# Performance work log

Measured on AMD Instinct MI355X. Metric: run time of the kernel, lower is better.

## Reference

```python
import math
import jax, jax.numpy as jnp
import numpy as np

S = 16384          # number of tokens
M = 1024           # model_dim
E = 64             # num_experts
CAPACITY_FACTOR = 1.0
MIN_CAPACITY = 8


def setup_inputs() -> dict:
    key = jax.random.key(0)
    kx, kw = jax.random.split(key)
    x = jax.random.normal(kx, (S, M), dtype=jnp.float32)
    wg_weight = jax.random.normal(kw, (E, M), dtype=jnp.float32) * 0.02  # torch Linear weight [out, in]
    return {"x": x, "wg_weight": wg_weight}


def reference(x, wg_weight):
    s, _ = x.shape
    e = wg_weight.shape[0]
    # gate linear (no bias), fp32 as in the torch module
    logits = jnp.einsum('sm,em->se', x, wg_weight)
    gates = jax.nn.softmax(logits, axis=1)

    # capacity (static: shapes + python floats)
    capacity = int(math.ceil(s / e * CAPACITY_FACTOR))
    capacity = max(capacity, MIN_CAPACITY)

    # top-1 expert per token
    indices1_s = jnp.argmax(gates, axis=1)                      # [s]
    mask1 = jax.nn.one_hot(indices1_s, e, dtype=jnp.int32)      # [s, e]
    exp_counts = jnp.sum(mask1, axis=0)                         # [e]

    alpha = jnp.max(gates, axis=1, keepdims=True)               # [s, 1]

    # load-balancing aux loss
    me = jnp.mean(gates, axis=0)
    ce = jnp.mean(mask1.astype(jnp.float32), axis=0)
    l_aux = jnp.sum(me * ce) * e

    # random tie-break for capacity selection (use_rts=True)
    rts_key = jax.random.key(42)
    mask1_rand = mask1.astype(jnp.float32) * jax.random.uniform(rts_key, (s, e), dtype=jnp.float32)

    # keep top-`capacity` tokens per expert (topk along token dim)
    top_idx = jax.lax.top_k(mask1_rand.T, capacity)[1].T        # [capacity, e]
    keep = jnp.zeros((s, e), dtype=jnp.int32).at[top_idx, jnp.arange(e)[None, :]].set(1)
    mask1 = mask1 * keep

    # slot assignment within each expert's capacity buffer
    locations1 = jnp.cumsum(mask1, axis=0) - 1                  # [s, e]
    locations1_s = jnp.sum(locations1 * mask1, axis=1)          # [s]

    mask1_float = mask1.astype(jnp.float32)
    gates = gates * mask1_float
    locations1_sc = jax.nn.one_hot(locations1_s, capacity, dtype=jnp.float32)  # [s, c]

    combine_weights = jnp.einsum('se,sc->sec', gates, locations1_sc)           # [s, e, c]
    dispatch_mask = combine_weights.astype(bool)

    return (l_aux, combine_weights, dispatch_mask, exp_counts, alpha)
```

## Files before the change

### kernel.cpp

```cpp
#include <hip/hip_runtime.h>
#include <stdint.h>

#define S_TOK 16384
#define MDIM  1024
#define NEXP  64
#define CAP   256

static constexpr size_t SEC    = (size_t)S_TOK * NEXP * CAP;
static constexpr size_t CW_OFF = 1;
static constexpr size_t DM_OFF = 1 + SEC;
static constexpr size_t EC_OFF = 1 + 2 * SEC;
static constexpr size_t AL_OFF = EC_OFF + NEXP;

__device__ __forceinline__ uint32_t rotl32(uint32_t x, int n) {
  return (x << n) | (x >> (32 - n));
}

__device__ float jax_u01(uint32_t i) {
  const uint32_t half = (uint32_t)(S_TOK * NEXP / 2);
  uint32_t x0, x1;
  const bool hi = (i >= half);
  if (hi) { x0 = i - half; x1 = i; } else { x0 = i; x1 = i + half; }
  const uint32_t ks0 = 0u;
  const uint32_t ks1 = 42u;
  const uint32_t ks2 = 0x1BD11BDAu ^ ks0 ^ ks1;
  x0 += ks0; x1 += ks1;
#define TF_R(r) { x0 += x1; x1 = rotl32(x1, (r)); x1 ^= x0; }
  TF_R(13) TF_R(15) TF_R(26) TF_R(6)
  x0 += ks1; x1 += ks2 + 1u;
  TF_R(17) TF_R(29) TF_R(16) TF_R(24)
  x0 += ks2; x1 += ks0 + 2u;
  TF_R(13) TF_R(15) TF_R(26) TF_R(6)
  x0 += ks0; x1 += ks1 + 3u;
  TF_R(17) TF_R(29) TF_R(16) TF_R(24)
  x0 += ks1; x1 += ks2 + 4u;
  TF_R(13) TF_R(15) TF_R(26) TF_R(6)
  x0 += ks2; x1 += ks0 + 5u;
#undef TF_R
  const uint32_t bits = hi ? x1 : x0;
  return __uint_as_float((bits >> 9) | 0x3F800000u) - 1.0f;
}

__global__ __launch_bounds__(256) void k_gate(
    const float* __restrict__ x, const float* __restrict__ wg,
    float* __restrict__ out,
    int* __restrict__ expert_ws, float* __restrict__ uval_ws,
    float* __restrict__ alpha_ws, float* __restrict__ colsum_ws,
    int* __restrict__ counts_ws)
{
  __shared__ float xs[64][68];
  __shared__ float wsh[64][68];

  const int tid  = threadIdx.x;
  const int tok0 = blockIdx.x * 64;
  const int tr   = tid >> 4;
  const int tc   = tid & 15;

  float acc[4][4] = {};

  for (int kc = 0; kc < MDIM; kc += 64) {
    __syncthreads();
#pragma unroll
    for (int i = 0; i < 4; ++i) {
      const int r = (tid >> 4) + 16 * i;
      const int f = tid & 15;
      const float4 xv = *(const float4*)(x  + (size_t)(tok0 + r) * MDIM + kc + f * 4);
      *(float4*)(&xs[r][f * 4]) = xv;
      const float4 wv = *(const float4*)(wg + (size_t)r * MDIM + kc + f * 4);
      const int fs = f ^ ((r >> 2) & 7);
      *(float4*)(&wsh[r][fs * 4]) = wv;
    }
    __syncthreads();
#pragma unroll
    for (int k4 = 0; k4 < 16; ++k4) {
      float4 a[4], b[4];
#pragma unroll
      for (int i = 0; i < 4; ++i)
        a[i] = *(const float4*)(&xs[tr * 4 + i][k4 * 4]);
#pragma unroll
      for (int j = 0; j < 4; ++j) {
        const int e  = tc * 4 + j;
        const int fs = k4 ^ ((e >> 2) & 7);
        b[j] = *(const float4*)(&wsh[e][fs * 4]);
      }
#pragma unroll
      for (int i = 0; i < 4; ++i)
#pragma unroll
        for (int j = 0; j < 4; ++j)
          acc[i][j] += a[i].x * b[j].x + a[i].y * b[j].y +
                       a[i].z * b[j].z + a[i].w * b[j].w;
    }
  }

  __syncthreads();
#pragma unroll
  for (int i = 0; i < 4; ++i)
#pragma unroll
    for (int j = 0; j < 4; ++j)
      xs[tr * 4 + i][tc * 4 + j] = acc[i][j];
  __syncthreads();

  if (tid < 64) {
    const int t = tid;
    float mx = -3.0e38f; int am = 0;
    for (int e = 0; e < NEXP; ++e) {
      const float v = xs[t][e];
      if (v > mx) { mx = v; am = e; }
    }
    float sum = 0.f;
    for (int e = 0; e < NEXP; ++e) {
      const float g = expf(xs[t][e] - mx);
      xs[t][e] = g;
      sum += g;
    }
    const float inv = 1.0f / sum;
    for (int e = 0; e < NEXP; ++e) xs[t][e] *= inv;

    const int s = tok0 + t;
    expert_ws[s] = am;
    alpha_ws[s]  = inv;
    out[AL_OFF + s] = inv;
    uval_ws[s] = jax_u01((uint32_t)s * (uint32_t)NEXP + (uint32_t)am);
    atomicAdd(&counts_ws[am], 1);
  }
  __syncthreads();

  if (tid < 64) {
    float s = 0.f;
    for (int t = 0; t < 64; ++t) s += xs[t][tid];
    colsum_ws[(size_t)blockIdx.x * 64 + tid] = s;
  }
}

__global__ __launch_bounds__(256) void k_select(
    const int* __restrict__ expert_ws, const float* __restrict__ uval_ws,
    const float* __restrict__ alpha_ws, float* __restrict__ out)
{
  __shared__ float su[1024];
  __shared__ int   sidx[1024];
  __shared__ int   skept[1024];
  __shared__ int   scnt;

  const int e   = blockIdx.x;
  const int tid = threadIdx.x;
  if (tid == 0) scnt = 0;
  __syncthreads();

  for (int s = tid; s < S_TOK; s += 256) {
    if (expert_ws[s] == e) {
      const int p = atomicAdd(&scnt, 1);
      if (p < 1024) { su[p] = uval_ws[s]; sidx[p] = s; }
    }
  }
  __syncthreads();
  const int n = min(scnt, 1024);

  for (int t = tid; t < n; t += 256) {
    int keep = 1;
    if (n > CAP) {
      const float ut = su[t];
      const int   it = sidx[t];
      int r = 0;
      for (int j = 0; j < n; ++j) {
        const float uj = su[j];
        r += (uj > ut) || (uj == ut && sidx[j] < it);
      }
      keep = (r < CAP);
    }
    skept[t] = keep;
  }
  __syncthreads();

  for (int t = tid; t < n; t += 256) {
    if (!skept[t]) continue;
    const int it = sidx[t];
    int slot = 0;
    for (int j = 0; j < n; ++j) slot += (skept[j] && (sidx[j] < it));
    const size_t base = CW_OFF + ((size_t)it * NEXP + e) * CAP + (size_t)slot;
    out[base]       = alpha_ws[it];
    out[base + SEC] = 1.0f;
  }
}

__global__ __launch_bounds__(64) void k_final(
    const float* __restrict__ colsum_ws, const int* __restrict__ counts_ws,
    float* __restrict__ out)
{
  const int e = threadIdx.x;
  float s = 0.f;
  for (int b = 0; b < 256; ++b) s += colsum_ws[(size_t)b * 64 + e];
  const float me = s / (float)S_TOK;
  const int   cnt = counts_ws[e];
  const float ce = (float)cnt / (float)S_TOK;
  out[EC_OFF + e] = (float)cnt;
  float v = me * ce;
#pragma unroll
  for (int off = 32; off > 0; off >>= 1) v += __shfl_down(v, off, 64);
  if (e == 0) out[0] = v * (float)NEXP;
}

extern "C" void kernel_launch(void* const* d_in, const int* in_sizes, int n_in,
                              void* d_out, int out_size, void* d_ws, size_t ws_size,
                              hipStream_t stream)
{
  const float* x  = (const float*)d_in[0];
  const float* wg = (const float*)d_in[1];
  float* out = (float*)d_out;

  char* ws = (char*)d_ws;
  int*   expert_ws = (int*)  (ws + 0);
  float* uval_ws   = (float*)(ws + 65536);
  float* alpha_ws  = (float*)(ws + 131072);
  float* colsum_ws = (float*)(ws + 196608);
  int*   counts_ws = (int*)  (ws + 262144);

  hipMemsetAsync(d_out, 0, (size_t)out_size * sizeof(float), stream);
  hipMemsetAsync(counts_ws, 0, NEXP * sizeof(int), stream);

  k_gate  <<<S_TOK / 64, 256, 0, stream>>>(x, wg, out, expert_ws, uval_ws,
                                           alpha_ws, colsum_ws, counts_ws);
  k_select<<<NEXP,       256, 0, stream>>>(expert_ws, uval_ws, alpha_ws, out);
  k_final <<<1,           64, 0, stream>>>(colsum_ws, counts_ws, out);
}
```

Before: 489.4 us.

## Replace full output memset and scatter with a single streaming dense write kernel

Drops the hipMemsetAsync of the whole output and the scattered writes. k_select now only records each token's flat slot index, and a new k_write kernel streams every row of combine_weights and dispatch_mask once with nontemporal vector stores, putting the value in place at the kept slot. Expert counts are taken from k_select's per-expert tally instead of global atomics, and the aux-loss reduction is folded into k_write. This removes one extra pass over the roughly 2 GB output, at the cost of handling the misaligned row offset with scalar edge stores.

Measured after the change: 741.0 us. +51.4%, slower.

```diff
diff --git a/kernel.cpp b/kernel.cpp
--- a/kernel.cpp
+++ b/kernel.cpp
@@ -8,9 +8,10 @@
 
 static constexpr size_t SEC    = (size_t)S_TOK * NEXP * CAP;
 static constexpr size_t CW_OFF = 1;
-static constexpr size_t DM_OFF = 1 + SEC;
 static constexpr size_t EC_OFF = 1 + 2 * SEC;
 static constexpr size_t AL_OFF = EC_OFF + NEXP;
+
+typedef float floatx4 __attribute__((ext_vector_type(4)));
 
 __device__ __forceinline__ uint32_t rotl32(uint32_t x, int n) {
   return (x << n) | (x >> (32 - n));
@@ -45,8 +46,7 @@
     const float* __restrict__ x, const float* __restrict__ wg,
     float* __restrict__ out,
     int* __restrict__ expert_ws, float* __restrict__ uval_ws,
-    float* __restrict__ alpha_ws, float* __restrict__ colsum_ws,
-    int* __restrict__ counts_ws)
+    float* __restrict__ alpha_ws, float* __restrict__ colsum_ws)
 {
   __shared__ float xs[64][68];
   __shared__ float wsh[64][68];
@@ -121,7 +121,6 @@
     alpha_ws[s]  = inv;
     out[AL_OFF + s] = inv;
     uval_ws[s] = jax_u01((uint32_t)s * (uint32_t)NEXP + (uint32_t)am);
-    atomicAdd(&counts_ws[am], 1);
   }
   __syncthreads();
 
@@ -134,7 +133,8 @@
 
 __global__ __launch_bounds__(256) void k_select(
     const int* __restrict__ expert_ws, const float* __restrict__ uval_ws,
-    const float* __restrict__ alpha_ws, float* __restrict__ out)
+    int* __restrict__ slotj_ws, int* __restrict__ counts_ws,
+    float* __restrict__ out)
 {
   __shared__ float su[1024];
   __shared__ int   sidx[1024];
@@ -154,6 +154,11 @@
   }
   __syncthreads();
   const int n = min(scnt, 1024);
+
+  if (tid == 0) {
+    counts_ws[e] = scnt;
+    out[EC_OFF + e] = (float)scnt;
+  }
 
   for (int t = tid; t < n; t += 256) {
     int keep = 1;
@@ -172,31 +177,55 @@
   __syncthreads();
 
   for (int t = tid; t < n; t += 256) {
-    if (!skept[t]) continue;
     const int it = sidx[t];
-    int slot = 0;
-    for (int j = 0; j < n; ++j) slot += (skept[j] && (sidx[j] < it));
-    const size_t base = CW_OFF + ((size_t)it * NEXP + e) * CAP + (size_t)slot;
-    out[base]       = alpha_ws[it];
-    out[base + SEC] = 1.0f;
-  }
-}
-
-__global__ __launch_bounds__(64) void k_final(
+    int sj = -1;
+    if (skept[t]) {
+      int slot = 0;
+      for (int j = 0; j < n; ++j) slot += (skept[j] && (sidx[j] < it));
+      sj = e * CAP + slot;
+    }
+    slotj_ws[it] = sj;
+  }
+}
+
+__global__ __launch_bounds__(256) void k_write(
+    const int* __restrict__ slotj_ws, const float* __restrict__ alpha_ws,
     const float* __restrict__ colsum_ws, const int* __restrict__ counts_ws,
     float* __restrict__ out)
 {
-  const int e = threadIdx.x;
-  float s = 0.f;
-  for (int b = 0; b < 256; ++b) s += colsum_ws[(size_t)b * 64 + e];
-  const float me = s / (float)S_TOK;
-  const int   cnt = counts_ws[e];
-  const float ce = (float)cnt / (float)S_TOK;
-  out[EC_OFF + e] = (float)cnt;
-  float v = me * ce;
-#pragma unroll
-  for (int off = 32; off > 0; off >>= 1) v += __shfl_down(v, off, 64);
-  if (e == 0) out[0] = v * (float)NEXP;
+  const int bid = blockIdx.x;
+  const int tid = threadIdx.x;
+  const int s   = bid & (S_TOK - 1);
+  const int r   = bid >> 14;
+
+  const size_t f0 = CW_OFF + (size_t)r * SEC + (size_t)s * 16384;
+  const int    tj = slotj_ws[s];
+  const float  val = r ? 1.0f : alpha_ws[s];
+
+  if (tid < 3)       out[f0 + tid]   = (tj == tid)   ? val : 0.0f;
+  else if (tid == 3) out[f0 + 16383] = (tj == 16383) ? val : 0.0f;
+
+  float* const rowp = out + f0 + 3;
+#pragma unroll 4
+  for (int q = tid; q < 4095; q += 256) {
+    const int jbase = 3 + q * 4;
+    floatx4 v = (floatx4)(0.f);
+    const int d = tj - jbase;
+    if ((unsigned)d < 4u) v[d] = val;
+    __builtin_nontemporal_store(v, (floatx4*)(rowp + q * 4));
+  }
+
+  if (bid == 0 && tid < 64) {
+    const int e = tid;
+    float cs = 0.f;
+    for (int b = 0; b < 256; ++b) cs += colsum_ws[(size_t)b * 64 + e];
+    const float me = cs / (float)S_TOK;
+    const float ce = (float)counts_ws[e] / (float)S_TOK;
+    float v = me * ce;
+#pragma unroll
+    for (int off = 32; off > 0; off >>= 1) v += __shfl_down(v, off, 64);
+    if (e == 0) out[0] = v * (float)NEXP;
+  }
 }
 
 extern "C" void kernel_launch(void* const* d_in, const int* in_sizes, int n_in,
@@ -213,12 +242,12 @@
   float* alpha_ws  = (float*)(ws + 131072);
   float* colsum_ws = (float*)(ws + 196608);
   int*   counts_ws = (int*)  (ws + 262144);
-
-  hipMemsetAsync(d_out, 0, (size_t)out_size * sizeof(float), stream);
-  hipMemsetAsync(counts_ws, 0, NEXP * sizeof(int), stream);
+  int*   slotj_ws  = (int*)  (ws + 262400);
 
   k_gate  <<<S_TOK / 64, 256, 0, stream>>>(x, wg, out, expert_ws, uval_ws,
-                                           alpha_ws, colsum_ws, counts_ws);
-  k_select<<<NEXP,       256, 0, stream>>>(expert_ws, uval_ws, alpha_ws, out);
-  k_final <<<1,           64, 0, stream>>>(colsum_ws, counts_ws, out);
-}
+                                           alpha_ws, colsum_ws);
+  k_select<<<NEXP,       256, 0, stream>>>(expert_ws, uval_ws, slotj_ws,
+                                           counts_ws, out);
+  k_write <<<2 * S_TOK,  256, 0, stream>>>(slotj_ws, alpha_ws, colsum_ws,
+                                           counts_ws, out);
+}
```

## Fuse output zero-fill into gate kernel and derive expert counts in select

Applied to the files above, without the earlier changes.

Drops the full-output hipMemsetAsync and the counts memset. The gate kernel gets extra blocks that zero the combine and dispatch regions with aligned float4 stores, so the fill runs alongside the gating GEMM blocks. Per-expert counts are now written by k_select from its per-expert gather count rather than by global atomics. The zero-fill stays bound by memory bandwidth, so any gain depends on overlapping it with the GEMM, on saving a launch, and on the custom fill matching the bandwidth of the driver memset.

Measured after the change: 533.6 us. 9.0% more time.

```diff
diff --git a/kernel.cpp b/kernel.cpp
--- a/kernel.cpp
+++ b/kernel.cpp
@@ -8,9 +8,11 @@
 
 static constexpr size_t SEC    = (size_t)S_TOK * NEXP * CAP;
 static constexpr size_t CW_OFF = 1;
-static constexpr size_t DM_OFF = 1 + SEC;
 static constexpr size_t EC_OFF = 1 + 2 * SEC;
 static constexpr size_t AL_OFF = EC_OFF + NEXP;
+
+static constexpr int    NFILLB = 32768;
+static constexpr size_t NQ4    = 134217727;
 
 __device__ __forceinline__ uint32_t rotl32(uint32_t x, int n) {
   return (x << n) | (x >> (32 - n));
@@ -41,17 +43,34 @@
   return __uint_as_float((bits >> 9) | 0x3F800000u) - 1.0f;
 }
 
-__global__ __launch_bounds__(256) void k_gate(
+__global__ __launch_bounds__(256) void k_gate_fill(
     const float* __restrict__ x, const float* __restrict__ wg,
     float* __restrict__ out,
     int* __restrict__ expert_ws, float* __restrict__ uval_ws,
-    float* __restrict__ alpha_ws, float* __restrict__ colsum_ws,
-    int* __restrict__ counts_ws)
+    float* __restrict__ alpha_ws, float* __restrict__ colsum_ws)
 {
   __shared__ float xs[64][68];
   __shared__ float wsh[64][68];
 
-  const int tid  = threadIdx.x;
+  const int tid = threadIdx.x;
+
+  if (blockIdx.x >= 256) {
+    const int fb = blockIdx.x - 256;
+    const size_t qbase = (size_t)fb * 4096;
+    const float4 z = make_float4(0.f, 0.f, 0.f, 0.f);
+    float* const p4 = out + 4;
+#pragma unroll 4
+    for (int i = 0; i < 16; ++i) {
+      const size_t q = qbase + (size_t)(i * 256 + tid);
+      if (q < NQ4) *(float4*)(p4 + q * 4) = z;
+    }
+    if (fb == 0) {
+      if (tid < 3)       out[1 + tid]          = 0.f;
+      else if (tid == 3) out[1 + 2 * SEC - 1]  = 0.f;
+    }
+    return;
+  }
+
   const int tok0 = blockIdx.x * 64;
   const int tr   = tid >> 4;
   const int tc   = tid & 15;
@@ -121,7 +140,6 @@
     alpha_ws[s]  = inv;
     out[AL_OFF + s] = inv;
     uval_ws[s] = jax_u01((uint32_t)s * (uint32_t)NEXP + (uint32_t)am);
-    atomicAdd(&counts_ws[am], 1);
   }
   __syncthreads();
 
@@ -134,7 +152,8 @@
 
 __global__ __launch_bounds__(256) void k_select(
     const int* __restrict__ expert_ws, const float* __restrict__ uval_ws,
-    const float* __restrict__ alpha_ws, float* __restrict__ out)
+    const float* __restrict__ alpha_ws, int* __restrict__ counts_ws,
+    float* __restrict__ out)
 {
   __shared__ float su[1024];
   __shared__ int   sidx[1024];
@@ -154,6 +173,11 @@
   }
   __syncthreads();
   const int n = min(scnt, 1024);
+
+  if (tid == 0) {
+    counts_ws[e] = scnt;
+    out[EC_OFF + e] = (float)scnt;
+  }
 
   for (int t = tid; t < n; t += 256) {
     int keep = 1;
@@ -190,9 +214,7 @@
   float s = 0.f;
   for (int b = 0; b < 256; ++b) s += colsum_ws[(size_t)b * 64 + e];
   const float me = s / (float)S_TOK;
-  const int   cnt = counts_ws[e];
-  const float ce = (float)cnt / (float)S_TOK;
-  out[EC_OFF + e] = (float)cnt;
+  const float ce = (float)counts_ws[e] / (float)S_TOK;
   float v = me * ce;
 #pragma unroll
   for (int off = 32; off > 0; off >>= 1) v += __shfl_down(v, off, 64);
@@ -214,11 +236,9 @@
   float* colsum_ws = (float*)(ws + 196608);
   int*   counts_ws = (int*)  (ws + 262144);
 
-  hipMemsetAsync(d_out, 0, (size_t)out_size * sizeof(float), stream);
-  hipMemsetAsync(counts_ws, 0, NEXP * sizeof(int), stream);
-
-  k_gate  <<<S_TOK / 64, 256, 0, stream>>>(x, wg, out, expert_ws, uval_ws,
-                                           alpha_ws, colsum_ws, counts_ws);
-  k_select<<<NEXP,       256, 0, stream>>>(expert_ws, uval_ws, alpha_ws, out);
-  k_final <<<1,           64, 0, stream>>>(colsum_ws, counts_ws, out);
-}
+  k_gate_fill<<<256 + NFILLB, 256, 0, stream>>>(x, wg, out, expert_ws, uval_ws,
+                                                alpha_ws, colsum_ws);
+  k_select   <<<NEXP,         256, 0, stream>>>(expert_ws, uval_ws, alpha_ws,
+                                                counts_ws, out);
+  k_final    <<<1,             64, 0, stream>>>(colsum_ws, counts_ws, out);
+}
```
